# Kernel tuning notes

Measured on AMD Instinct MI355X. Metric: run time of the kernel, lower is better.

The kernel has to match this reference:

```python
import jax, jax.numpy as jnp
import numpy as np

DIM, HEADS, HD, FFN = 1536, 12, 128, 8960
B, F, H, W = 1, 4, 20, 32
S = F * H * W          # 2560 latent tokens
L2 = 512               # text context length
EPS = 1e-6


def _ln(x):
    m = jnp.mean(x, -1, keepdims=True)
    v = jnp.mean(jnp.square(x - m), -1, keepdims=True)
    return (x - m) * jax.lax.rsqrt(v + EPS)


def _rms(x, g):
    return x * jax.lax.rsqrt(jnp.mean(jnp.square(x), -1, keepdims=True) + EPS) * g


def _dyn_quant(x):
    # per-token symmetric int8 dynamic activation quantization (A8, dynamic input scale)
    s = jnp.maximum(jnp.max(jnp.abs(x), -1, keepdims=True) / 127.0, 1e-8)
    q = jnp.clip(jnp.round(x / s), -127.0, 127.0)
    return q, s, jnp.sum(q, -1)   # sum_input used for asymmetric-weight zero-point correction


def _quant_w(w):
    # per-output-channel asymmetric int8 weight quantization (weight_sym=False)
    wmin = jnp.min(w, 1, keepdims=True)
    wmax = jnp.max(w, 1, keepdims=True)
    s = jnp.maximum((wmax - wmin) / 255.0, 1e-8)
    zp = jnp.round(-128.0 - wmin / s)
    qw = jnp.clip(jnp.round(w / s) + zp, -128.0, 127.0)
    return qw, s[:, 0], zp[:, 0]


def _w8a8(qx, s_x, sum_qx, w, b):
    # y = s_x * s_w * (qx @ (qw - zp)^T) + b = s_x*s_w*(qx@qw^T - zp*sum(qx)) + b
    qw, sw, zp = _quant_w(w)
    acc = jnp.einsum('bsi,oi->bso', qx, qw) - sum_qx[..., None] * zp
    return acc * s_x * sw + b


def _rope(x, fr, f, h, w):
    # x: [B,S,N,D] with S == f*h*w; fr: [1024, D//2] complex rope table
    Bn, Sn, N, D = x.shape
    c = D // 2
    s0 = c - 2 * (c // 3)
    fF = jnp.broadcast_to(fr[:f, :s0].reshape(f, 1, 1, s0), (f, h, w, s0))
    fH = jnp.broadcast_to(fr[:h, s0:s0 + c // 3].reshape(1, h, 1, c // 3), (f, h, w, c // 3))
    fW = jnp.broadcast_to(fr[:w, s0 + c // 3:].reshape(1, 1, w, c // 3), (f, h, w, c // 3))
    fi = jnp.concatenate([fF, fH, fW], -1).reshape(1, f * h * w, 1, c)
    xr = x.reshape(Bn, Sn, N, c, 2)
    xc = jax.lax.complex(xr[..., 0], xr[..., 1]) * fi
    return jnp.stack([jnp.real(xc), jnp.imag(xc)], -1).reshape(Bn, Sn, N, D)


def _attn(q, k, v, k_lens):
    scale = 1.0 / jnp.sqrt(jnp.float32(q.shape[-1]))
    scores = jnp.einsum('bqnd,bknd->bnqk', q, k) * scale
    mask = jnp.arange(k.shape[1])[None, None, None, :] < k_lens[:, None, None, None]
    p = jax.nn.softmax(jnp.where(mask, scores, -1e30), -1)
    return jnp.einsum('bnqk,bknd->bqnd', p, v)


def _forward(x, e, freqs, context, modulation,
             wq, bq, wk, bk, wv, bv, wo, bo, gq, gk, n3_w, n3_b,
             cwq, cbq, cwk, cbk, cwv, cbv, cwo, cbo, cgq, cgk,
             w1, b1, w2, b2, f, h, w, seq_lens, context_lens):
    fr = jax.lax.complex(freqs[..., 0], freqs[..., 1])
    em = modulation + e  # [B,6,C]
    sm, sc, gm, smlp, scmlp, gmlp = [em[:, i:i + 1] for i in range(6)]
    Bn, Sn, C = x.shape
    # --- self attention: fused norm+modulation then shared per-token int8 quant for q/k/v ---
    h1 = _ln(x) * (1.0 + sc) + sm
    qx, s_x, sum_qx = _dyn_quant(h1)
    q = _rms(_w8a8(qx, s_x, sum_qx, wq, bq), gq).reshape(Bn, Sn, HEADS, HD)
    k = _rms(_w8a8(qx, s_x, sum_qx, wk, bk), gk).reshape(Bn, Sn, HEADS, HD)
    v = _w8a8(qx, s_x, sum_qx, wv, bv).reshape(Bn, Sn, HEADS, HD)
    q = _rope(q, fr, f, h, w)
    k = _rope(k, fr, f, h, w)
    y = _attn(q, k, v, seq_lens).reshape(Bn, Sn, C) @ wo.T + bo
    x = x + y * gm
    # --- cross attention (fp16/fp path in the original; use_kernel[1]=False) ---
    hx = _ln(x) * n3_w + n3_b
    cq = _rms(hx @ cwq.T + cbq, cgq).reshape(Bn, Sn, HEADS, HD)
    ck = _rms(context @ cwk.T + cbk, cgk).reshape(Bn, L2, HEADS, HD)
    cv = (context @ cwv.T + cbv).reshape(Bn, L2, HEADS, HD)
    y = _attn(cq, ck, cv, context_lens).reshape(Bn, Sn, C) @ cwo.T + cbo
    x = x + y
    # --- FFN with modulation (use_kernel[2]=False) ---
    h2 = _ln(x) * (1.0 + scmlp) + smlp
    y = jax.nn.gelu(h2 @ w1.T + b1, approximate=True) @ w2.T + b2
    return x + y * gmlp


def setup_inputs():
    key = jax.random.key(0)
    ks = jax.random.split(key, 16)

    def P(i, shape, s=0.02):
        return jax.random.normal(ks[i], shape, jnp.float32) * s

    x = jax.random.normal(ks[0], (B, S, DIM), jnp.float32)
    e = jax.random.normal(ks[1], (B, 6, DIM), jnp.float32)
    context = jax.random.normal(ks[2], (B, L2, DIM), jnp.float32)
    seq_lens = jnp.array([S], jnp.int32)
    grid_sizes = jnp.array([[F, H, W]], jnp.int32)
    context_lens = jnp.array([L2], jnp.int32)
    c = HD // 2
    pos = np.arange(1024, dtype=np.float64)[:, None]
    theta = 1.0 / (10000.0 ** (np.arange(c, dtype=np.float64) / c))
    ang = pos * theta
    freqs = jnp.asarray(np.stack([np.cos(ang), np.sin(ang)], -1), jnp.float32)
    z = lambda n: jnp.zeros((n,), jnp.float32)
    o = lambda n: jnp.ones((n,), jnp.float32)
    return dict(x=x, e=e, seq_lens=seq_lens, grid_sizes=grid_sizes, freqs=freqs,
                context=context, context_lens=context_lens,
                modulation=P(3, (1, 6, DIM), 1.0 / DIM ** 0.5),
                wq=P(4, (DIM, DIM)), bq=z(DIM), wk=P(5, (DIM, DIM)), bk=z(DIM),
                wv=P(6, (DIM, DIM)), bv=z(DIM), wo=P(7, (DIM, DIM)), bo=z(DIM),
                gq=o(DIM), gk=o(DIM), n3_w=o(DIM), n3_b=z(DIM),
                cwq=P(8, (DIM, DIM)), cbq=z(DIM), cwk=P(9, (DIM, DIM)), cbk=z(DIM),
                cwv=P(10, (DIM, DIM)), cbv=z(DIM), cwo=P(11, (DIM, DIM)), cbo=z(DIM),
                cgq=o(DIM), cgk=o(DIM),
                w1=P(12, (FFN, DIM)), b1=z(FFN), w2=P(13, (DIM, FFN)), b2=z(DIM))


def reference(x, e, seq_lens, grid_sizes, freqs, context, context_lens, modulation,
              wq, bq, wk, bk, wv, bv, wo, bo, gq, gk, n3_w, n3_b,
              cwq, cbq, cwk, cbk, cwv, cbv, cwo, cbo, cgq, cgk,
              w1, b1, w2, b2):
    f, h, w = int(grid_sizes[0, 0]), int(grid_sizes[0, 1]), int(grid_sizes[0, 2])
    return _forward(x, e, freqs, context, modulation,
                    wq, bq, wk, bk, wv, bv, wo, bo, gq, gk, n3_w, n3_b,
                    cwq, cbq, cwk, cbk, cwv, cbv, cwo, cbo, cgq, cgk,
                    w1, b1, w2, b2, f, h, w, seq_lens, context_lens)
```

## Files before the change

kernel.cpp:

```cpp
#include <hip/hip_runtime.h>
#include <stdint.h>


typedef unsigned short u16;
typedef __bf16 bf16x8 __attribute__((ext_vector_type(8)));
typedef float f32x4 __attribute__((ext_vector_type(4)));

#define DEV __device__ __forceinline__

DEV u16 f2b(float f) {
  uint32_t u = __float_as_uint(f);
  u += 0x7fffu + ((u >> 16) & 1u);
  return (u16)(u >> 16);
}

DEV float gelu_tanh(float v) {
  float u = 0.7978845608028654f * (v + 0.044715f * v * v * v);
  return 0.5f * v * (1.0f + tanhf(u));
}

DEV float bred_sum(float v, float* scr) {
  #pragma unroll
  for (int o = 32; o; o >>= 1) v += __shfl_down(v, o, 64);
  if ((threadIdx.x & 63) == 0) scr[threadIdx.x >> 6] = v;
  __syncthreads();
  v = scr[0] + scr[1] + scr[2] + scr[3];
  __syncthreads();
  return v;
}
DEV float bred_max(float v, float* scr) {
  #pragma unroll
  for (int o = 32; o; o >>= 1) v = fmaxf(v, __shfl_down(v, o, 64));
  if ((threadIdx.x & 63) == 0) scr[threadIdx.x >> 6] = v;
  __syncthreads();
  v = fmaxf(fmaxf(scr[0], scr[1]), fmaxf(scr[2], scr[3]));
  __syncthreads();
  return v;
}
DEV float bred_min(float v, float* scr) {
  #pragma unroll
  for (int o = 32; o; o >>= 1) v = fminf(v, __shfl_down(v, o, 64));
  if ((threadIdx.x & 63) == 0) scr[threadIdx.x >> 6] = v;
  __syncthreads();
  v = fminf(fminf(scr[0], scr[1]), fminf(scr[2], scr[3]));
  __syncthreads();
  return v;
}

__global__ __launch_bounds__(256) void pack_kernel(
    const float* __restrict__ e, const float* __restrict__ mod,
    const float* __restrict__ cbk, const float* __restrict__ cbv,
    float* __restrict__ em, float* __restrict__ bckv) {
  int i = blockIdx.x * 256 + threadIdx.x;
  if (i < 9216) em[i] = e[i] + mod[i];
  if (i < 3072) bckv[i] = (i < 1536) ? cbk[i] : cbv[i - 1536];
}

__global__ __launch_bounds__(256) void cvt_bf16_kernel(
    const float* __restrict__ in, u16* __restrict__ out, int n4) {
  int stride = gridDim.x * 256;
  for (int i = blockIdx.x * 256 + threadIdx.x; i < n4; i += stride) {
    float4 v = ((const float4*)in)[i];
    uint2 r;
    r.x = (uint32_t)f2b(v.x) | ((uint32_t)f2b(v.y) << 16);
    r.y = (uint32_t)f2b(v.z) | ((uint32_t)f2b(v.w) << 16);
    ((uint2*)out)[i] = r;
  }
}

__global__ __launch_bounds__(256) void ln_quant_kernel(
    const float* __restrict__ x, const float* __restrict__ em,
    u16* __restrict__ qx, float* __restrict__ sx, float* __restrict__ sumq) {
  __shared__ float scr[4];
  const int row = blockIdx.x, tid = threadIdx.x;
  const float* xr = x + (size_t)row * 1536;
  float v[6], s = 0.f, s2 = 0.f;
  #pragma unroll
  for (int t = 0; t < 6; t++) { v[t] = xr[tid + t * 256]; s += v[t]; s2 += v[t] * v[t]; }
  s = bred_sum(s, scr); s2 = bred_sum(s2, scr);
  float mean = s / 1536.f;
  float var = s2 / 1536.f - mean * mean;
  float inv = rsqrtf(var + 1e-6f);
  float hv[6], amax = 0.f;
  #pragma unroll
  for (int t = 0; t < 6; t++) {
    int i = tid + t * 256;
    hv[t] = (v[t] - mean) * inv * (1.f + em[1536 + i]) + em[i];
    amax = fmaxf(amax, fabsf(hv[t]));
  }
  amax = bred_max(amax, scr);
  float sxv = fmaxf(amax / 127.f, 1e-8f);
  float qs = 0.f;
  #pragma unroll
  for (int t = 0; t < 6; t++) {
    int i = tid + t * 256;
    float q = fminf(fmaxf(rintf(hv[t] / sxv), -127.f), 127.f);
    qs += q;
    qx[(size_t)row * 1536 + i] = f2b(q);
  }
  qs = bred_sum(qs, scr);
  if (tid == 0) { sx[row] = sxv; sumq[row] = qs; }
}

__global__ __launch_bounds__(256) void quantw_kernel(
    const float* __restrict__ wq, const float* __restrict__ wk, const float* __restrict__ wv,
    const float* __restrict__ bq, const float* __restrict__ bk, const float* __restrict__ bv,
    u16* __restrict__ qw, float* __restrict__ sw, float* __restrict__ zp, float* __restrict__ ball) {
  __shared__ float scr[4];
  const int row = blockIdx.x, tid = threadIdx.x;
  const int sel = (row >= 3072) ? 2 : (row >= 1536 ? 1 : 0);
  const int r = row - sel * 1536;
  const float* w = sel == 0 ? wq : (sel == 1 ? wk : wv);
  const float* bb = sel == 0 ? bq : (sel == 1 ? bk : bv);
  const float* wr = w + (size_t)r * 1536;
  float v[6], mn = 1e30f, mx = -1e30f;
  #pragma unroll
  for (int t = 0; t < 6; t++) { v[t] = wr[tid + t * 256]; mn = fminf(mn, v[t]); mx = fmaxf(mx, v[t]); }
  mn = bred_min(mn, scr); mx = bred_max(mx, scr);
  float s = fmaxf((mx - mn) / 255.f, 1e-8f);
  float z = rintf(-128.f - mn / s);
  #pragma unroll
  for (int t = 0; t < 6; t++) {
    int i = tid + t * 256;
    float q = fminf(fmaxf(rintf(v[t] / s) + z, -128.f), 127.f);
    qw[(size_t)row * 1536 + i] = f2b(q);
  }
  if (tid == 0) { sw[row] = s; zp[row] = z; ball[row] = bb[r]; }
}

template<int BM, int BN, int EP>
__global__ __launch_bounds__(256) void gemm_bt_kernel(
    const u16* __restrict__ A, const u16* __restrict__ B, void* __restrict__ Cout,
    int N, int K, const float* __restrict__ bias,
    const float* __restrict__ sxp, const float* __restrict__ sumqp,
    const float* __restrict__ swp, const float* __restrict__ zpp,
    const float* __restrict__ gp, const float* __restrict__ residp) {
  constexpr int WMI = BM / 32, WNI = BN / 32;
  constexpr int ALD = (BM * 32) / 2048, BLD = (BN * 32) / 2048;
  __shared__ __align__(16) u16 As[BM * 32];
  __shared__ __align__(16) u16 Bs[BN * 32];
  const int tid = threadIdx.x;
  const int wave = tid >> 6, lane = tid & 63;
  const int wm = wave >> 1, wn = wave & 1;
  const int quad = lane >> 4, l16 = lane & 15;
  const int m0 = blockIdx.y * BM, n0 = blockIdx.x * BN;

  f32x4 acc[WMI][WNI];
  #pragma unroll
  for (int i = 0; i < WMI; i++)
    #pragma unroll
    for (int j = 0; j < WNI; j++) acc[i][j] = (f32x4){0.f, 0.f, 0.f, 0.f};

  for (int k0 = 0; k0 < K; k0 += 32) {
    #pragma unroll
    for (int i = 0; i < ALD; i++) {
      int flat = (i * 256 + tid) * 8;
      int row = flat >> 5, col = flat & 31;
      uint4 t = *(const uint4*)(A + (size_t)(m0 + row) * K + k0 + col);
      *(uint4*)&As[flat] = t;
    }
    #pragma unroll
    for (int i = 0; i < BLD; i++) {
      int flat = (i * 256 + tid) * 8;
      int row = flat >> 5, col = flat & 31;
      uint4 t = *(const uint4*)(B + (size_t)(n0 + row) * K + k0 + col);
      *(uint4*)&Bs[flat] = t;
    }
    __syncthreads();
    bf16x8 af[WMI], bfv[WNI];
    #pragma unroll
    for (int mi = 0; mi < WMI; mi++)
      af[mi] = *(const bf16x8*)&As[(wm * (WMI * 16) + mi * 16 + l16) * 32 + quad * 8];
    #pragma unroll
    for (int ni = 0; ni < WNI; ni++)
      bfv[ni] = *(const bf16x8*)&Bs[(wn * (WNI * 16) + ni * 16 + l16) * 32 + quad * 8];
    #pragma unroll
    for (int mi = 0; mi < WMI; mi++)
      #pragma unroll
      for (int ni = 0; ni < WNI; ni++)
        acc[mi][ni] = __builtin_amdgcn_mfma_f32_16x16x32_bf16(af[mi], bfv[ni], acc[mi][ni], 0, 0, 0);
    __syncthreads();
  }
  #pragma unroll
  for (int mi = 0; mi < WMI; mi++) {
    #pragma unroll
    for (int ni = 0; ni < WNI; ni++) {
      int col = n0 + wn * (WNI * 16) + ni * 16 + l16;
      #pragma unroll
      for (int r = 0; r < 4; r++) {
        int row = m0 + wm * (WMI * 16) + mi * 16 + quad * 4 + r;
        float v = acc[mi][ni][r];
        size_t idx = (size_t)row * N + col;
        if constexpr (EP == 0) {
          ((float*)Cout)[idx] = v + bias[col];
        } else if constexpr (EP == 1) {
          v = (v - sumqp[row] * zpp[col]) * (sxp[row] * swp[col]) + bias[col];
          ((float*)Cout)[idx] = v;
        } else if constexpr (EP == 2) {
          v += bias[col];
          if (gp) v *= gp[col];
          ((float*)Cout)[idx] = v + residp[idx];
        } else {
          ((u16*)Cout)[idx] = f2b(gelu_tanh(v + bias[col]));
        }
      }
    }
  }
}

__global__ __launch_bounds__(256) void rmsrope_b_kernel(
    const float* __restrict__ qkv, u16* __restrict__ qkvb,
    const float* __restrict__ gq, const float* __restrict__ gk,
    const float* __restrict__ freqs, const int* __restrict__ gsz) {
  __shared__ float scr[4];
  const int row = blockIdx.x, tid = threadIdx.x;
  const float* base = qkv + (size_t)row * 4608;
  u16* ob = qkvb + (size_t)row * 4608;
  const int gh = gsz[1], gw = gsz[2];
  const int hw = gh * gw;
  const int fi = row / hw, rem = row - fi * hw;
  const int hi = rem / gw, wi = rem - hi * gw;
  #pragma unroll
  for (int part = 0; part < 2; part++) {
    const float* p = base + part * 1536;
    u16* o = ob + part * 1536;
    const float* g = part ? gk : gq;
    const float sc = part ? 1.f : 0.08838834764831845f;
    float v[6], s2 = 0.f;
    #pragma unroll
    for (int t = 0; t < 6; t++) { v[t] = p[tid + t * 256]; s2 += v[t] * v[t]; }
    s2 = bred_sum(s2, scr);
    float inv = rsqrtf(s2 / 1536.f + 1e-6f);
    #pragma unroll
    for (int t = 0; t < 3; t++) {
      int pr = tid + t * 256;
      int c = pr & 63;
      int frow = (c < 22) ? fi : (c < 43 ? hi : wi);
      const float* fr = freqs + ((size_t)frow * 64 + c) * 2;
      float cv = fr[0], sv = fr[1];
      float x0 = p[2 * pr] * inv * g[2 * pr];
      float x1 = p[2 * pr + 1] * inv * g[2 * pr + 1];
      o[2 * pr] = f2b((x0 * cv - x1 * sv) * sc);
      o[2 * pr + 1] = f2b((x0 * sv + x1 * cv) * sc);
    }
  }
  #pragma unroll
  for (int t = 0; t < 6; t++) {
    int i = tid + t * 256;
    ob[3072 + i] = f2b(base[3072 + i]);
  }
}

__global__ __launch_bounds__(256) void rms_bf16_kernel(
    const float* __restrict__ X, u16* __restrict__ O, const float* __restrict__ g,
    int ldi, int ldo, float scale) {
  __shared__ float scr[4];
  const int row = blockIdx.x, tid = threadIdx.x;
  const float* xr = X + (size_t)row * ldi;
  u16* orow = O + (size_t)row * ldo;
  float v[6], s2 = 0.f;
  #pragma unroll
  for (int t = 0; t < 6; t++) { v[t] = xr[tid + t * 256]; s2 += v[t] * v[t]; }
  s2 = bred_sum(s2, scr);
  float inv = rsqrtf(s2 / 1536.f + 1e-6f) * scale;
  #pragma unroll
  for (int t = 0; t < 6; t++) {
    int i = tid + t * 256;
    orow[i] = f2b(v[t] * inv * g[i]);
  }
}

__global__ __launch_bounds__(256) void vtrans_kernel(
    const float* __restrict__ V, int ld, u16* __restrict__ Vt, int Skv) {
  __shared__ u16 T[64 * 136];
  const int h = blockIdx.y, k0 = blockIdx.x * 64, tid = threadIdx.x;
  #pragma unroll
  for (int i = 0; i < 8; i++) {
    int f4 = i * 256 + tid;
    int row = f4 >> 5, c4 = f4 & 31;
    float4 v = *(const float4*)(V + (size_t)(k0 + row) * ld + h * 128 + c4 * 4);
    ushort4 b;
    b.x = f2b(v.x); b.y = f2b(v.y); b.z = f2b(v.z); b.w = f2b(v.w);
    *(ushort4*)&T[row * 136 + c4 * 4] = b;
  }
  __syncthreads();
  #pragma unroll
  for (int i = 0; i < 4; i++) {
    int f8 = i * 256 + tid;
    int hd = f8 >> 3, kc = f8 & 7;
    u16 tmp[8];
    #pragma unroll
    for (int j = 0; j < 8; j++) tmp[j] = T[(kc * 8 + j) * 136 + hd];
    *(uint4*)(Vt + ((size_t)h * 128 + hd) * Skv + k0 + kc * 8) = *(const uint4*)tmp;
  }
}

__global__ __launch_bounds__(256) void fattn_kernel(
    const u16* __restrict__ Q, int ldq, const u16* __restrict__ Kg, int ldk,
    const u16* __restrict__ Vtg, u16* __restrict__ O, int ldo,
    const int* __restrict__ klen_ptr, int kmax) {
  __shared__ __align__(16) u16 Qs[64 * 136];
  __shared__ __align__(16) u16 Ks[64 * 136];
  __shared__ __align__(16) u16 Vt[128 * 72];
  __shared__ __align__(16) u16 Pt[4][16 * 72];
  const int tid = threadIdx.x, wave = tid >> 6, lane = tid & 63;
  const int quad = lane >> 4, l16 = lane & 15;
  const int h = blockIdx.y;
  const int q0 = blockIdx.x * 64;
  int klen = klen_ptr[0]; if (klen > kmax) klen = kmax;
  const u16* vbase = Vtg + (size_t)h * 128 * kmax;

  #pragma unroll
  for (int i = 0; i < 4; i++) {
    int c8 = i * 256 + tid;
    int row = c8 >> 4, cc = (c8 & 15) * 8;
    *(uint4*)&Qs[row * 136 + cc] = *(const uint4*)(Q + (size_t)(q0 + row) * ldq + h * 128 + cc);
  }
  __syncthreads();
  bf16x8 qf[4];
  #pragma unroll
  for (int s = 0; s < 4; s++)
    qf[s] = *(const bf16x8*)&Qs[(wave * 16 + l16) * 136 + s * 32 + quad * 8];

  float m_r[4] = {-1e30f, -1e30f, -1e30f, -1e30f};
  float l_r[4] = {0.f, 0.f, 0.f, 0.f};
  f32x4 oacc[8];
  #pragma unroll
  for (int n8 = 0; n8 < 8; n8++) oacc[n8] = (f32x4){0.f, 0.f, 0.f, 0.f};

  const int ktiles = (klen + 63) >> 6;
  for (int kt = 0; kt < ktiles; kt++) {
    const int k0 = kt * 64;
    __syncthreads();
    #pragma unroll
    for (int i = 0; i < 4; i++) {
      int c8 = i * 256 + tid;
      int row = c8 >> 4, cc = (c8 & 15) * 8;
      *(uint4*)&Ks[row * 136 + cc] = *(const uint4*)(Kg + (size_t)(k0 + row) * ldk + h * 128 + cc);
    }
    #pragma unroll
    for (int i = 0; i < 4; i++) {
      int f8 = i * 256 + tid;
      int hd = f8 >> 3, kc = f8 & 7;
      *(uint4*)&Vt[hd * 72 + kc * 8] = *(const uint4*)(vbase + (size_t)hd * kmax + k0 + kc * 8);
    }
    __syncthreads();
    f32x4 sacc[4];
    #pragma unroll
    for (int ni = 0; ni < 4; ni++) sacc[ni] = (f32x4){0.f, 0.f, 0.f, 0.f};
    #pragma unroll
    for (int ni = 0; ni < 4; ni++)
      #pragma unroll
      for (int s = 0; s < 4; s++) {
        bf16x8 kf = *(const bf16x8*)&Ks[(ni * 16 + l16) * 136 + s * 32 + quad * 8];
        sacc[ni] = __builtin_amdgcn_mfma_f32_16x16x32_bf16(qf[s], kf, sacc[ni], 0, 0, 0);
      }
    float alpha_r[4];
    #pragma unroll
    for (int r = 0; r < 4; r++) {
      float mx = -1e30f;
      #pragma unroll
      for (int ni = 0; ni < 4; ni++) {
        int col = k0 + ni * 16 + l16;
        float sv = (col < klen) ? sacc[ni][r] : -1e30f;
        sacc[ni][r] = sv;
        mx = fmaxf(mx, sv);
      }
      #pragma unroll
      for (int off = 1; off < 16; off <<= 1) mx = fmaxf(mx, __shfl_xor(mx, off, 64));
      float mnew = fmaxf(m_r[r], mx);
      float alpha = __expf(m_r[r] - mnew);
      float rsum = 0.f;
      float pv[4];
      #pragma unroll
      for (int ni = 0; ni < 4; ni++) {
        float p = __expf(sacc[ni][r] - mnew);
        pv[ni] = p;
        rsum += p;
      }
      #pragma unroll
      for (int off = 1; off < 16; off <<= 1) rsum += __shfl_xor(rsum, off, 64);
      l_r[r] = l_r[r] * alpha + rsum;
      m_r[r] = mnew;
      alpha_r[r] = alpha;
      #pragma unroll
      for (int ni = 0; ni < 4; ni++)
        Pt[wave][(quad * 4 + r) * 72 + ni * 16 + l16] = f2b(pv[ni]);
    }
    #pragma unroll
    for (int n8 = 0; n8 < 8; n8++)
      #pragma unroll
      for (int r = 0; r < 4; r++) oacc[n8][r] *= alpha_r[r];
    #pragma unroll
    for (int s2 = 0; s2 < 2; s2++) {
      bf16x8 pf = *(const bf16x8*)&Pt[wave][l16 * 72 + s2 * 32 + quad * 8];
      #pragma unroll
      for (int n8 = 0; n8 < 8; n8++) {
        bf16x8 vf = *(const bf16x8*)&Vt[(n8 * 16 + l16) * 72 + s2 * 32 + quad * 8];
        oacc[n8] = __builtin_amdgcn_mfma_f32_16x16x32_bf16(pf, vf, oacc[n8], 0, 0, 0);
      }
    }
  }
  float rl[4];
  #pragma unroll
  for (int r = 0; r < 4; r++) rl[r] = 1.f / l_r[r];
  #pragma unroll
  for (int n8 = 0; n8 < 8; n8++)
    #pragma unroll
    for (int r = 0; r < 4; r++) {
      int row = q0 + wave * 16 + quad * 4 + r;
      O[(size_t)row * ldo + h * 128 + n8 * 16 + l16] = f2b(oacc[n8][r] * rl[r]);
    }
}

__global__ __launch_bounds__(256) void ln_affine_kernel(
    const float* __restrict__ X, u16* __restrict__ O,
    const float* __restrict__ w, const float* __restrict__ b, float addone) {
  __shared__ float scr[4];
  const int row = blockIdx.x, tid = threadIdx.x;
  const float* xr = X + (size_t)row * 1536;
  float v[6], s = 0.f, s2 = 0.f;
  #pragma unroll
  for (int t = 0; t < 6; t++) { v[t] = xr[tid + t * 256]; s += v[t]; s2 += v[t] * v[t]; }
  s = bred_sum(s, scr); s2 = bred_sum(s2, scr);
  float mean = s / 1536.f;
  float inv = rsqrtf(s2 / 1536.f - mean * mean + 1e-6f);
  #pragma unroll
  for (int t = 0; t < 6; t++) {
    int i = tid + t * 256;
    O[(size_t)row * 1536 + i] = f2b((v[t] - mean) * inv * (addone + w[i]) + b[i]);
  }
}

extern "C" void kernel_launch(void* const* d_in, const int* in_sizes, int n_in,
                              void* d_out, int out_size, void* d_ws, size_t ws_size,
                              hipStream_t stream) {
  (void)in_sizes; (void)n_in; (void)out_size; (void)ws_size;
  const int S = 2560, D = 1536, L2C = 512, FF = 8960, ND = 4608, CKV = 3072;

  const float* x = (const float*)d_in[0];
  const float* e = (const float*)d_in[1];
  const int* seq_lens = (const int*)d_in[2];
  const int* grid_sz = (const int*)d_in[3];
  const float* freqs = (const float*)d_in[4];
  const float* context = (const float*)d_in[5];
  const int* ctx_lens = (const int*)d_in[6];
  const float* modulation = (const float*)d_in[7];
  const float* wq = (const float*)d_in[8];  const float* bq = (const float*)d_in[9];
  const float* wk = (const float*)d_in[10]; const float* bk = (const float*)d_in[11];
  const float* wv = (const float*)d_in[12]; const float* bv = (const float*)d_in[13];
  const float* wo = (const float*)d_in[14]; const float* bo = (const float*)d_in[15];
  const float* gq = (const float*)d_in[16]; const float* gk = (const float*)d_in[17];
  const float* n3w = (const float*)d_in[18]; const float* n3b = (const float*)d_in[19];
  const float* cwq = (const float*)d_in[20]; const float* cbq = (const float*)d_in[21];
  const float* cwk = (const float*)d_in[22]; const float* cbk = (const float*)d_in[23];
  const float* cwv = (const float*)d_in[24]; const float* cbv = (const float*)d_in[25];
  const float* cwo = (const float*)d_in[26]; const float* cbo = (const float*)d_in[27];
  const float* cgq = (const float*)d_in[28]; const float* cgk = (const float*)d_in[29];
  const float* w1 = (const float*)d_in[30]; const float* b1 = (const float*)d_in[31];
  const float* w2 = (const float*)d_in[32]; const float* b2 = (const float*)d_in[33];

  char* wsb = (char*)d_ws;
  size_t off = 0;
  auto alloc = [&](size_t bytes) -> void* {
    void* r = wsb + off;
    off += (bytes + 255) & ~(size_t)255;
    return r;
  };
  float* em   = (float*)alloc((size_t)6 * D * 4);
  float* bckv = (float*)alloc((size_t)CKV * 4);
  float* ball = (float*)alloc((size_t)ND * 4);
  float* sx   = (float*)alloc((size_t)S * 4);
  float* sumq = (float*)alloc((size_t)S * 4);
  float* sw   = (float*)alloc((size_t)ND * 4);
  float* zp   = (float*)alloc((size_t)ND * 4);
  u16* qx     = (u16*)alloc((size_t)S * D * 2);
  u16* qw     = (u16*)alloc((size_t)ND * D * 2);
  float* qkv  = (float*)alloc((size_t)S * ND * 4);
  u16* qkvb   = (u16*)alloc((size_t)S * ND * 2);
  u16* attnb  = (u16*)alloc((size_t)S * D * 2);
  u16* hx     = (u16*)alloc((size_t)S * D * 2);
  float* cq   = (float*)alloc((size_t)S * D * 4);
  float* ckv  = (float*)alloc((size_t)L2C * CKV * 4);
  u16* ctxb   = (u16*)alloc((size_t)L2C * D * 2);
  u16* cattn  = (u16*)alloc((size_t)S * D * 2);
  u16* wo_b   = (u16*)alloc((size_t)D * D * 2);
  u16* cwq_b  = (u16*)alloc((size_t)D * D * 2);
  u16* cwkv_b = (u16*)alloc((size_t)2 * D * D * 2);
  u16* cwo_b  = (u16*)alloc((size_t)D * D * 2);
  u16* w1_b   = (u16*)alloc((size_t)FF * D * 2);
  u16* w2_b   = (u16*)alloc((size_t)D * FF * 2);
  u16* h3 = (u16*)qkv;
  u16* h2 = attnb;
  u16* vtg = qw;
  u16* cvtg = qx;
  u16* cqb = hx;
  u16* ckvb = ctxb;
  float* x2 = cq;
  float* x1 = (float*)d_out;
  float* outp = (float*)d_out;

  auto cvt = [&](const float* in, u16* op, size_t n) {
    int n4 = (int)(n / 4);
    int blocks = (n4 + 255) / 256; if (blocks > 4096) blocks = 4096;
    cvt_bf16_kernel<<<blocks, 256, 0, stream>>>(in, op, n4);
  };

  pack_kernel<<<36, 256, 0, stream>>>(e, modulation, cbk, cbv, em, bckv);
  cvt(wo, wo_b, (size_t)D * D);
  cvt(cwq, cwq_b, (size_t)D * D);
  cvt(cwk, cwkv_b, (size_t)D * D);
  cvt(cwv, cwkv_b + (size_t)D * D, (size_t)D * D);
  cvt(cwo, cwo_b, (size_t)D * D);
  cvt(w1, w1_b, (size_t)FF * D);
  cvt(w2, w2_b, (size_t)D * FF);
  cvt(context, ctxb, (size_t)L2C * D);

  ln_quant_kernel<<<S, 256, 0, stream>>>(x, em, qx, sx, sumq);
  quantw_kernel<<<ND, 256, 0, stream>>>(wq, wk, wv, bq, bk, bv, qw, sw, zp, ball);

  gemm_bt_kernel<128, 128, 1><<<dim3(ND / 128, S / 128), 256, 0, stream>>>(
      qx, qw, qkv, ND, D, ball, sx, sumq, sw, zp, nullptr, nullptr);

  rmsrope_b_kernel<<<S, 256, 0, stream>>>(qkv, qkvb, gq, gk, freqs, grid_sz);
  vtrans_kernel<<<dim3(S / 64, 12), 256, 0, stream>>>(qkv + 3072, ND, vtg, S);

  fattn_kernel<<<dim3(S / 64, 12), 256, 0, stream>>>(
      qkvb, ND, qkvb + 1536, ND, vtg, attnb, D, seq_lens, S);

  gemm_bt_kernel<64, 64, 2><<<dim3(D / 64, S / 64), 256, 0, stream>>>(
      attnb, wo_b, x1, D, D, bo, nullptr, nullptr, nullptr, nullptr, em + 2 * D, x);

  ln_affine_kernel<<<S, 256, 0, stream>>>(x1, hx, n3w, n3b, 0.f);

  gemm_bt_kernel<64, 64, 0><<<dim3(D / 64, S / 64), 256, 0, stream>>>(
      hx, cwq_b, cq, D, D, cbq, nullptr, nullptr, nullptr, nullptr, nullptr, nullptr);
  gemm_bt_kernel<64, 64, 0><<<dim3(CKV / 64, L2C / 64), 256, 0, stream>>>(
      ctxb, cwkv_b, ckv, CKV, D, bckv, nullptr, nullptr, nullptr, nullptr, nullptr, nullptr);

  rms_bf16_kernel<<<S, 256, 0, stream>>>(cq, cqb, cgq, D, D, 0.08838834764831845f);
  rms_bf16_kernel<<<L2C, 256, 0, stream>>>(ckv, ckvb, cgk, CKV, D, 1.f);
  vtrans_kernel<<<dim3(L2C / 64, 12), 256, 0, stream>>>(ckv + 1536, CKV, cvtg, L2C);

  fattn_kernel<<<dim3(S / 64, 12), 256, 0, stream>>>(
      cqb, D, ckvb, D, cvtg, cattn, D, ctx_lens, L2C);

  gemm_bt_kernel<64, 64, 2><<<dim3(D / 64, S / 64), 256, 0, stream>>>(
      cattn, cwo_b, x2, D, D, cbo, nullptr, nullptr, nullptr, nullptr, nullptr, x1);

  ln_affine_kernel<<<S, 256, 0, stream>>>(x2, h2, em + 4 * D, em + 3 * D, 1.f);

  gemm_bt_kernel<128, 128, 3><<<dim3(FF / 128, S / 128), 256, 0, stream>>>(
      h2, w1_b, h3, FF, D, b1, nullptr, nullptr, nullptr, nullptr, nullptr, nullptr);

  gemm_bt_kernel<64, 64, 2><<<dim3(D / 64, S / 64), 256, 0, stream>>>(
      h3, w2_b, outp, D, FF, b2, nullptr, nullptr, nullptr, nullptr, em + 5 * D, x2);
}
```

Before: 1.016 ms.

## Load GEMM tiles directly into LDS with swizzle and unify 128x128 tiles

Replaces register-staged global-to-LDS copies in the GEMM with direct global_load_lds transfers, and adds an XOR-style chunk swizzle to the LDS layout to avoid bank conflicts on fragment reads. It also fixes every GEMM to 128x128 tiles, including the D-by-D projections and the FFN down projection that used 64x64. Larger tiles raise reuse per block but cut the number of blocks for the 1536-wide outputs (240 blocks), which may underfill the GPU. The direct LDS load assumes the builtin's per-lane addressing matches the swizzled layout.

```diff
diff --git a/kernel.cpp b/kernel.cpp
--- a/kernel.cpp
+++ b/kernel.cpp
@@ -17,6 +17,12 @@
 DEV float gelu_tanh(float v) {
   float u = 0.7978845608028654f * (v + 0.044715f * v * v * v);
   return 0.5f * v * (1.0f + tanhf(u));
+}
+
+DEV void gl_lds16(const u16* g, u16* l) {
+  __builtin_amdgcn_global_load_lds(
+      (const __attribute__((address_space(1))) void*)g,
+      (__attribute__((address_space(3))) void*)l, 16, 0, 0);
 }
 
 DEV float bred_sum(float v, float* scr) {
@@ -128,67 +134,68 @@
   if (tid == 0) { sw[row] = s; zp[row] = z; ball[row] = bb[r]; }
 }
 
-template<int BM, int BN, int EP>
+template<int EP>
 __global__ __launch_bounds__(256) void gemm_bt_kernel(
     const u16* __restrict__ A, const u16* __restrict__ B, void* __restrict__ Cout,
     int N, int K, const float* __restrict__ bias,
     const float* __restrict__ sxp, const float* __restrict__ sumqp,
     const float* __restrict__ swp, const float* __restrict__ zpp,
     const float* __restrict__ gp, const float* __restrict__ residp) {
-  constexpr int WMI = BM / 32, WNI = BN / 32;
-  constexpr int ALD = (BM * 32) / 2048, BLD = (BN * 32) / 2048;
-  __shared__ __align__(16) u16 As[BM * 32];
-  __shared__ __align__(16) u16 Bs[BN * 32];
+  __shared__ __align__(16) u16 As[128 * 32];
+  __shared__ __align__(16) u16 Bs[128 * 32];
   const int tid = threadIdx.x;
   const int wave = tid >> 6, lane = tid & 63;
   const int wm = wave >> 1, wn = wave & 1;
   const int quad = lane >> 4, l16 = lane & 15;
-  const int m0 = blockIdx.y * BM, n0 = blockIdx.x * BN;
-
-  f32x4 acc[WMI][WNI];
-  #pragma unroll
-  for (int i = 0; i < WMI; i++)
-    #pragma unroll
-    for (int j = 0; j < WNI; j++) acc[i][j] = (f32x4){0.f, 0.f, 0.f, 0.f};
+  const int m0 = blockIdx.y * 128, n0 = blockIdx.x * 128;
+
+  int srow[2], scol[2];
+  #pragma unroll
+  for (int i = 0; i < 2; i++) {
+    int row = (wave * 2 + i) * 16 + (lane >> 2);
+    int chunk = ((lane & 3) - (row >> 1)) & 3;
+    srow[i] = row; scol[i] = chunk * 8;
+  }
+
+  f32x4 acc[4][4];
+  #pragma unroll
+  for (int i = 0; i < 4; i++)
+    #pragma unroll
+    for (int j = 0; j < 4; j++) acc[i][j] = (f32x4){0.f, 0.f, 0.f, 0.f};
 
   for (int k0 = 0; k0 < K; k0 += 32) {
     #pragma unroll
-    for (int i = 0; i < ALD; i++) {
-      int flat = (i * 256 + tid) * 8;
-      int row = flat >> 5, col = flat & 31;
-      uint4 t = *(const uint4*)(A + (size_t)(m0 + row) * K + k0 + col);
-      *(uint4*)&As[flat] = t;
-    }
-    #pragma unroll
-    for (int i = 0; i < BLD; i++) {
-      int flat = (i * 256 + tid) * 8;
-      int row = flat >> 5, col = flat & 31;
-      uint4 t = *(const uint4*)(B + (size_t)(n0 + row) * K + k0 + col);
-      *(uint4*)&Bs[flat] = t;
+    for (int i = 0; i < 2; i++) {
+      gl_lds16(A + (size_t)(m0 + srow[i]) * K + k0 + scol[i], &As[(wave * 2 + i) * 512]);
+      gl_lds16(B + (size_t)(n0 + srow[i]) * K + k0 + scol[i], &Bs[(wave * 2 + i) * 512]);
     }
     __syncthreads();
-    bf16x8 af[WMI], bfv[WNI];
-    #pragma unroll
-    for (int mi = 0; mi < WMI; mi++)
-      af[mi] = *(const bf16x8*)&As[(wm * (WMI * 16) + mi * 16 + l16) * 32 + quad * 8];
-    #pragma unroll
-    for (int ni = 0; ni < WNI; ni++)
-      bfv[ni] = *(const bf16x8*)&Bs[(wn * (WNI * 16) + ni * 16 + l16) * 32 + quad * 8];
-    #pragma unroll
-    for (int mi = 0; mi < WMI; mi++)
-      #pragma unroll
-      for (int ni = 0; ni < WNI; ni++)
+    bf16x8 af[4], bfv[4];
+    #pragma unroll
+    for (int mi = 0; mi < 4; mi++) {
+      int row = wm * 64 + mi * 16 + l16;
+      af[mi] = *(const bf16x8*)&As[row * 32 + (((quad + (row >> 1)) & 3) * 8)];
+    }
+    #pragma unroll
+    for (int ni = 0; ni < 4; ni++) {
+      int row = wn * 64 + ni * 16 + l16;
+      bfv[ni] = *(const bf16x8*)&Bs[row * 32 + (((quad + (row >> 1)) & 3) * 8)];
+    }
+    #pragma unroll
+    for (int mi = 0; mi < 4; mi++)
+      #pragma unroll
+      for (int ni = 0; ni < 4; ni++)
         acc[mi][ni] = __builtin_amdgcn_mfma_f32_16x16x32_bf16(af[mi], bfv[ni], acc[mi][ni], 0, 0, 0);
     __syncthreads();
   }
   #pragma unroll
-  for (int mi = 0; mi < WMI; mi++) {
-    #pragma unroll
-    for (int ni = 0; ni < WNI; ni++) {
-      int col = n0 + wn * (WNI * 16) + ni * 16 + l16;
+  for (int mi = 0; mi < 4; mi++) {
+    #pragma unroll
+    for (int ni = 0; ni < 4; ni++) {
+      int col = n0 + wn * 64 + ni * 16 + l16;
       #pragma unroll
       for (int r = 0; r < 4; r++) {
-        int row = m0 + wm * (WMI * 16) + mi * 16 + quad * 4 + r;
+        int row = m0 + wm * 64 + mi * 16 + quad * 4 + r;
         float v = acc[mi][ni][r];
         size_t idx = (size_t)row * N + col;
         if constexpr (EP == 0) {
@@ -519,7 +526,7 @@
   ln_quant_kernel<<<S, 256, 0, stream>>>(x, em, qx, sx, sumq);
   quantw_kernel<<<ND, 256, 0, stream>>>(wq, wk, wv, bq, bk, bv, qw, sw, zp, ball);
 
-  gemm_bt_kernel<128, 128, 1><<<dim3(ND / 128, S / 128), 256, 0, stream>>>(
+  gemm_bt_kernel<1><<<dim3(ND / 128, S / 128), 256, 0, stream>>>(
       qx, qw, qkv, ND, D, ball, sx, sumq, sw, zp, nullptr, nullptr);
 
   rmsrope_b_kernel<<<S, 256, 0, stream>>>(qkv, qkvb, gq, gk, freqs, grid_sz);
@@ -528,14 +535,14 @@
   fattn_kernel<<<dim3(S / 64, 12), 256, 0, stream>>>(
       qkvb, ND, qkvb + 1536, ND, vtg, attnb, D, seq_lens, S);
 
-  gemm_bt_kernel<64, 64, 2><<<dim3(D / 64, S / 64), 256, 0, stream>>>(
+  gemm_bt_kernel<2><<<dim3(D / 128, S / 128), 256, 0, stream>>>(
       attnb, wo_b, x1, D, D, bo, nullptr, nullptr, nullptr, nullptr, em + 2 * D, x);
 
   ln_affine_kernel<<<S, 256, 0, stream>>>(x1, hx, n3w, n3b, 0.f);
 
-  gemm_bt_kernel<64, 64, 0><<<dim3(D / 64, S / 64), 256, 0, stream>>>(
+  gemm_bt_kernel<0><<<dim3(D / 128, S / 128), 256, 0, stream>>>(
       hx, cwq_b, cq, D, D, cbq, nullptr, nullptr, nullptr, nullptr, nullptr, nullptr);
-  gemm_bt_kernel<64, 64, 0><<<dim3(CKV / 64, L2C / 64), 256, 0, stream>>>(
+  gemm_bt_kernel<0><<<dim3(CKV / 128, L2C / 128), 256, 0, stream>>>(
       ctxb, cwkv_b, ckv, CKV, D, bckv, nullptr, nullptr, nullptr, nullptr, nullptr, nullptr);
 
   rms_bf16_kernel<<<S, 256, 0, stream>>>(cq, cqb, cgq, D, D, 0.08838834764831845f);
@@ -545,14 +552,14 @@
   fattn_kernel<<<dim3(S / 64, 12), 256, 0, stream>>>(
       cqb, D, ckvb, D, cvtg, cattn, D, ctx_lens, L2C);
 
-  gemm_bt_kernel<64, 64, 2><<<dim3(D / 64, S / 64), 256, 0, stream>>>(
+  gemm_bt_kernel<2><<<dim3(D / 128, S / 128), 256, 0, stream>>>(
       cattn, cwo_b, x2, D, D, cbo, nullptr, nullptr, nullptr, nullptr, nullptr, x1);
 
   ln_affine_kernel<<<S, 256, 0, stream>>>(x2, h2, em + 4 * D, em + 3 * D, 1.f);
 
-  gemm_bt_kernel<128, 128, 3><<<dim3(FF / 128, S / 128), 256, 0, stream>>>(
+  gemm_bt_kernel<3><<<dim3(FF / 128, S / 128), 256, 0, stream>>>(
       h2, w1_b, h3, FF, D, b1, nullptr, nullptr, nullptr, nullptr, nullptr, nullptr);
 
-  gemm_bt_kernel<64, 64, 2><<<dim3(D / 64, S / 64), 256, 0, stream>>>(
+  gemm_bt_kernel<2><<<dim3(D / 128, S / 128), 256, 0, stream>>>(
       h3, w2_b, outp, D, FF, b2, nullptr, nullptr, nullptr, nullptr, em + 5 * D, x2);
 }
```

Measured after the change: 1.108 ms. +9.1%, slower.
